# Performance work log

Hardware: AMD Instinct MI355X
Metric: run time of the kernel (lower is better)

## Reference

```python
import jax, jax.numpy as jnp
import numpy as np

N_NODES = 131072
N_EDGES = 2097152
N_GRAPHS = 2048
IN_CH, HID, OUT = 12, 64, 4


def gcn_conv(x, W, b, src, dst, n_nodes):
    """PyG GCNConv: out = D^{-1/2} (A + I) D^{-1/2} (x W) + b.
    Degree computed at target nodes including self loops (edge_weight=1)."""
    h = x @ W  # [N, F_out]
    # degree with self loops: in-degree + 1
    deg = jax.ops.segment_sum(jnp.ones((src.shape[0],), x.dtype), dst,
                              num_segments=n_nodes) + 1.0
    dinv = jax.lax.rsqrt(deg)  # [N]
    norm = dinv[src] * dinv[dst]  # [E]
    # scatter-add messages from src to dst
    agg = jax.ops.segment_sum(h[src] * norm[:, None], dst, num_segments=n_nodes)
    # self-loop contribution: norm_ii = dinv[i]^2
    agg = agg + h * (dinv * dinv)[:, None]
    return agg + b


def global_mean_pool(x, batch, n_graphs):
    sums = jax.ops.segment_sum(x, batch, num_segments=n_graphs)
    cnt = jax.ops.segment_sum(jnp.ones((x.shape[0],), x.dtype), batch,
                              num_segments=n_graphs)
    return sums / jnp.maximum(cnt, 1.0)[:, None]


def setup_inputs() -> dict:
    key = jax.random.key(0)
    ks = jax.random.split(key, 9)
    x = jax.random.normal(ks[0], (N_NODES, IN_CH), dtype=jnp.float32)
    edge_index = jax.random.randint(ks[1], (2, N_EDGES), 0, N_NODES, dtype=jnp.int64)
    batch = jnp.sort(jax.random.randint(ks[2], (N_NODES,), 0, N_GRAPHS, dtype=jnp.int64))
    def glorot(k, shape):
        lim = np.sqrt(6.0 / (shape[0] + shape[1]))
        return jax.random.uniform(k, shape, jnp.float32, -lim, lim)
    return {
        "x": x,
        "edge_index": edge_index,
        "batch": batch,
        "W1": glorot(ks[3], (IN_CH, HID)),
        "b1": jnp.zeros((HID,), jnp.float32),
        "W2": glorot(ks[4], (HID, HID)),
        "b2": jnp.zeros((HID,), jnp.float32),
        "Wfc": glorot(ks[5], (HID, OUT)),
        "bfc": jnp.zeros((OUT,), jnp.float32),
    }


def reference(x, edge_index, batch, W1, b1, W2, b2, Wfc, bfc):
    src, dst = edge_index[0], edge_index[1]
    h = jax.nn.relu(gcn_conv(x, W1, b1, src, dst, N_NODES))
    h = jax.nn.relu(gcn_conv(h, W2, b2, src, dst, N_NODES))
    g = global_mean_pool(h, batch, N_GRAPHS)  # [n_graphs, HID]
    return jax.nn.sigmoid(g @ Wfc + bfc)  # [n_graphs, OUT]
```

## Files before the change

### kernel.cpp

```cpp
#include <hip/hip_runtime.h>
#include <hip/hip_bf16.h>


#define N_NODES 131072
#define N_EDGES 2097152
#define N_GRAPHS 2048
#define IN_CH 12
#define HID 64
#define OUT_CH 4
#define NBUCK 512
#define CHUNK 8192
#define STRIDE 4608
#define CSR_STRIDE 5120
#define CAP 5120

typedef float f32x2 __attribute__((ext_vector_type(2)));

__global__ __launch_bounds__(1024, 4)
void bucket_kernel(const int* __restrict__ src, const int* __restrict__ dst,
                   int* __restrict__ bucket_count, int* __restrict__ staged) {
    __shared__ int hist[NBUCK];
    __shared__ int lscan[NBUCK];
    __shared__ int gbase[NBUCK];
    __shared__ int cursor[NBUCK];
    __shared__ int sorted[CHUNK];
    int tid = threadIdx.x;
    int base = blockIdx.x * CHUNK;
    if (tid < NBUCK) { hist[tid] = 0; cursor[tid] = 0; }
    __syncthreads();
    int d8[8], s8[8];
#pragma unroll
    for (int k = 0; k < 8; k++) {
        int i = base + k * 1024 + tid;
        d8[k] = dst[i];
        s8[k] = src[i];
        atomicAdd(&hist[d8[k] >> 8], 1);
    }
    __syncthreads();
    if (tid < NBUCK) lscan[tid] = hist[tid];
    __syncthreads();
    for (int off = 1; off < NBUCK; off <<= 1) {
        int u = (tid < NBUCK && tid >= off) ? lscan[tid - off] : 0;
        __syncthreads();
        if (tid < NBUCK) lscan[tid] += u;
        __syncthreads();
    }
    if (tid < NBUCK) gbase[tid] = atomicAdd(&bucket_count[tid], hist[tid]);
    __syncthreads();
#pragma unroll
    for (int k = 0; k < 8; k++) {
        int b = d8[k] >> 8;
        int start = lscan[b] - hist[b];
        int p = start + atomicAdd(&cursor[b], 1);
        sorted[p] = ((d8[k] & 255) << 17) | s8[k];
    }
    __syncthreads();
    int wid = tid >> 6, lane = tid & 63;
    int g16 = lane >> 4, k16 = lane & 15;
    for (int b0 = wid * 4; b0 < NBUCK; b0 += 64) {
        int b = b0 + g16;
        int cb = hist[b];
        int lbase = lscan[b] - cb;
        int gb = b * STRIDE + gbase[b];
        for (int k = k16; k < cb; k += 16) staged[gb + k] = sorted[lbase + k];
    }
}

__global__ void build_kernel(const int* __restrict__ bucket_count, const int* __restrict__ staged,
                             int2* __restrict__ rowbounds, float* __restrict__ dinv,
                             int* __restrict__ csr, const float* __restrict__ x,
                             uint4* __restrict__ xb) {
    __shared__ int sl[STRIDE];
    __shared__ int image[CAP];
    __shared__ int cnt[256];
    __shared__ int scn[256];
    __shared__ int loff[256];
    __shared__ int cursor[256];
    __shared__ int totalS;
    int b = blockIdx.x;
    int tid = threadIdx.x;
    int count = bucket_count[b];
    const int* st = staged + b * STRIDE;
    cnt[tid] = 0;
    cursor[tid] = 0;
    for (int i = tid; i < count; i += 256) sl[i] = st[i];
    __syncthreads();
    for (int i = tid; i < count; i += 256) atomicAdd(&cnt[(sl[i] >> 17) & 255], 1);
    __syncthreads();
    int deg = cnt[tid];
    int degp = (deg + 3) & ~3;
    scn[tid] = degp;
    __syncthreads();
    for (int off = 1; off < 256; off <<= 1) {
        int u = (tid >= off) ? scn[tid - off] : 0;
        __syncthreads();
        scn[tid] += u;
        __syncthreads();
    }
    int lo = scn[tid] - degp;
    loff[tid] = lo;
    int nbase = (b << 8) + tid;
    int gb = b * CSR_STRIDE;
    rowbounds[nbase] = make_int2(gb + lo, gb + lo + degp);
    float dv = rsqrtf((float)deg + 1.0f);
    dinv[nbase] = dv;
    if (tid == 255) totalS = lo + degp;
    {
        const float* xp = x + nbase * IN_CH;
        unsigned o0 = (unsigned)__builtin_amdgcn_cvt_pk_fp8_f32(dv * xp[0], dv * xp[1], 0, false);
        o0 = (unsigned)__builtin_amdgcn_cvt_pk_fp8_f32(dv * xp[2], dv * xp[3], (int)o0, true);
        unsigned o1 = (unsigned)__builtin_amdgcn_cvt_pk_fp8_f32(dv * xp[4], dv * xp[5], 0, false);
        o1 = (unsigned)__builtin_amdgcn_cvt_pk_fp8_f32(dv * xp[6], dv * xp[7], (int)o1, true);
        unsigned o2 = (unsigned)__builtin_amdgcn_cvt_pk_fp8_f32(dv * xp[8], dv * xp[9], 0, false);
        o2 = (unsigned)__builtin_amdgcn_cvt_pk_fp8_f32(dv * xp[10], dv * xp[11], (int)o2, true);
        xb[nbase] = make_uint4(o0, o1, o2, 0);
    }
    if (b == 0 && tid == 0)
        xb[N_NODES] = make_uint4(0, 0, 0, 0);
    __syncthreads();
    for (int i = tid; i < count; i += 256) {
        int rec = sl[i];
        int s = rec & 0x1FFFF;
        int dq = (rec >> 17) & 255;
        int p = loff[dq] + atomicAdd(&cursor[dq], 1);
        int val = s << 6;
        if (p < CAP) image[p] = val;
        else csr[gb + p] = val;
    }
    __syncthreads();
    int padval = N_NODES << 6;
    for (int p = loff[tid] + deg; p < loff[tid] + degp; p++) {
        if (p < CAP) image[p] = padval;
        else csr[gb + p] = padval;
    }
    __syncthreads();
    int lim = totalS < CAP ? totalS : CAP;
    int* dstp = csr + gb;
    for (int i = tid; i < lim; i += 256) dstp[i] = image[i];
}

__device__ __forceinline__ void accq2(f32x2* a, uint2 u) {
    a[0] += __builtin_amdgcn_cvt_pk_f32_fp8((int)u.x, false);
    a[1] += __builtin_amdgcn_cvt_pk_f32_fp8((int)u.x, true);
    a[2] += __builtin_amdgcn_cvt_pk_f32_fp8((int)u.y, false);
    a[3] += __builtin_amdgcn_cvt_pk_f32_fp8((int)u.y, true);
}

__global__ __launch_bounds__(256, 6)
void w1w2_kernel(const int2* __restrict__ rowbounds, const int* __restrict__ csr,
                 const float* __restrict__ dinv, const unsigned char* __restrict__ xb,
                 const float* __restrict__ W1, const float* __restrict__ b1,
                 const float* __restrict__ W2, unsigned int* __restrict__ hout) {
    __shared__ float sA[64 * 13];
    __shared__ float sh1t[HID * 65];
    int tid = threadIdx.x;
    int node0 = blockIdx.x * 64;
    {
        int nl = tid >> 2;
        int node = node0 + nl;
        int p = tid & 1, boff = 8 * p;
        int2 rb = rowbounds[node];
        float dn = dinv[node];
        uint2 su = {0, 0};
        if (!(tid & 2)) su = *(const uint2*)(xb + node * 16 + boff);
        int len = rb.y - rb.x;
        int hlen = (len >> 3) << 2;
        int beg = (tid & 2) ? rb.x + hlen : rb.x;
        int end = (tid & 2) ? rb.y : rb.x + hlen;
        f32x2 a0[4] = {{0, 0}, {0, 0}, {0, 0}, {0, 0}};
        f32x2 a1[4] = {{0, 0}, {0, 0}, {0, 0}, {0, 0}};
        int j = beg;
        for (; j + 8 <= end; j += 8) {
            int4 ea = *(const int4*)(csr + j);
            int4 eb = *(const int4*)(csr + j + 4);
            uint2 u0 = *(const uint2*)(xb + (ea.x >> 2) + boff);
            uint2 u1 = *(const uint2*)(xb + (ea.y >> 2) + boff);
            uint2 u2 = *(const uint2*)(xb + (ea.z >> 2) + boff);
            uint2 u3 = *(const uint2*)(xb + (ea.w >> 2) + boff);
            uint2 u4 = *(const uint2*)(xb + (eb.x >> 2) + boff);
            uint2 u5 = *(const uint2*)(xb + (eb.y >> 2) + boff);
            uint2 u6 = *(const uint2*)(xb + (eb.z >> 2) + boff);
            uint2 u7 = *(const uint2*)(xb + (eb.w >> 2) + boff);
            accq2(a0, u0); accq2(a1, u1); accq2(a0, u2); accq2(a1, u3);
            accq2(a0, u4); accq2(a1, u5); accq2(a0, u6); accq2(a1, u7);
        }
        if (j < end) {
            int4 ea = *(const int4*)(csr + j);
            uint2 u0 = *(const uint2*)(xb + (ea.x >> 2) + boff);
            uint2 u1 = *(const uint2*)(xb + (ea.y >> 2) + boff);
            uint2 u2 = *(const uint2*)(xb + (ea.z >> 2) + boff);
            uint2 u3 = *(const uint2*)(xb + (ea.w >> 2) + boff);
            accq2(a0, u0); accq2(a1, u1); accq2(a0, u2); accq2(a1, u3);
        }
        f32x2 s0 = a0[0] + a1[0];
        f32x2 s1 = a0[1] + a1[1];
        f32x2 s2 = a0[2] + a1[2];
        f32x2 s3 = a0[3] + a1[3];
        s0[0] += __shfl_xor(s0[0], 2); s0[1] += __shfl_xor(s0[1], 2);
        s1[0] += __shfl_xor(s1[0], 2); s1[1] += __shfl_xor(s1[1], 2);
        s2[0] += __shfl_xor(s2[0], 2); s2[1] += __shfl_xor(s2[1], 2);
        s3[0] += __shfl_xor(s3[0], 2); s3[1] += __shfl_xor(s3[1], 2);
        if (!(tid & 2)) {
            s0 += __builtin_amdgcn_cvt_pk_f32_fp8((int)su.x, false);
            s1 += __builtin_amdgcn_cvt_pk_f32_fp8((int)su.x, true);
            s2 += __builtin_amdgcn_cvt_pk_f32_fp8((int)su.y, false);
            s3 += __builtin_amdgcn_cvt_pk_f32_fp8((int)su.y, true);
            float* dp = &sA[nl * 13 + 8 * p];
            dp[0] = dn * s0[0]; dp[1] = dn * s0[1];
            dp[2] = dn * s1[0]; dp[3] = dn * s1[1];
            if (p == 0) {
                dp[4] = dn * s2[0]; dp[5] = dn * s2[1];
                dp[6] = dn * s3[0]; dp[7] = dn * s3[1];
            }
        }
    }
    __syncthreads();
    int w = tid >> 6, c = tid & 63;
    float bc = b1[c];
    float wk[IN_CH];
#pragma unroll
    for (int k = 0; k < IN_CH; k++) wk[k] = W1[k * HID + c];
#pragma unroll
    for (int it = 0; it < 4; it++) {
        int n0 = w * 16 + it * 4;
        float a0 = bc, a1 = bc, a2 = bc, a3 = bc;
#pragma unroll
        for (int k = 0; k < IN_CH; k++) {
            float wv = wk[k];
            a0 += sA[(n0 + 0) * 13 + k] * wv;
            a1 += sA[(n0 + 1) * 13 + k] * wv;
            a2 += sA[(n0 + 2) * 13 + k] * wv;
            a3 += sA[(n0 + 3) * 13 + k] * wv;
        }
        float4 o = make_float4(fmaxf(a0, 0.0f), fmaxf(a1, 0.0f),
                               fmaxf(a2, 0.0f), fmaxf(a3, 0.0f));
        *(float4*)&sh1t[c * 65 + n0] = o;
    }
    __syncthreads();
    int nq = tid >> 4, c4 = (tid & 15) * 4;
    float4 a0 = {0, 0, 0, 0}, a1 = {0, 0, 0, 0}, a2 = {0, 0, 0, 0}, a3 = {0, 0, 0, 0};
#pragma unroll 4
    for (int k = 0; k < HID; k++) {
        float4 wv = *(const float4*)&W2[k * HID + c4];
        float4 hv = *(const float4*)&sh1t[k * 65 + nq * 4];
        a0.x += hv.x * wv.x; a0.y += hv.x * wv.y; a0.z += hv.x * wv.z; a0.w += hv.x * wv.w;
        a1.x += hv.y * wv.x; a1.y += hv.y * wv.y; a1.z += hv.y * wv.z; a1.w += hv.y * wv.w;
        a2.x += hv.z * wv.x; a2.y += hv.z * wv.y; a2.z += hv.z * wv.z; a2.w += hv.z * wv.w;
        a3.x += hv.w * wv.x; a3.y += hv.w * wv.y; a3.z += hv.w * wv.z; a3.w += hv.w * wv.w;
    }
    int nb = node0 + nq * 4;
    float dv0 = dinv[nb + 0], dv1 = dinv[nb + 1], dv2 = dinv[nb + 2], dv3 = dinv[nb + 3];
    unsigned int p0 = (unsigned int)__builtin_amdgcn_cvt_pk_fp8_f32(dv0 * a0.x, dv0 * a0.y, 0, false);
    p0 = (unsigned int)__builtin_amdgcn_cvt_pk_fp8_f32(dv0 * a0.z, dv0 * a0.w, (int)p0, true);
    unsigned int p1 = (unsigned int)__builtin_amdgcn_cvt_pk_fp8_f32(dv1 * a1.x, dv1 * a1.y, 0, false);
    p1 = (unsigned int)__builtin_amdgcn_cvt_pk_fp8_f32(dv1 * a1.z, dv1 * a1.w, (int)p1, true);
    unsigned int p2 = (unsigned int)__builtin_amdgcn_cvt_pk_fp8_f32(dv2 * a2.x, dv2 * a2.y, 0, false);
    p2 = (unsigned int)__builtin_amdgcn_cvt_pk_fp8_f32(dv2 * a2.z, dv2 * a2.w, (int)p2, true);
    unsigned int p3 = (unsigned int)__builtin_amdgcn_cvt_pk_fp8_f32(dv3 * a3.x, dv3 * a3.y, 0, false);
    p3 = (unsigned int)__builtin_amdgcn_cvt_pk_fp8_f32(dv3 * a3.z, dv3 * a3.w, (int)p3, true);
    int cl = c4 >> 2;
    hout[(nb + 0) * 16 + cl] = p0;
    hout[(nb + 1) * 16 + cl] = p1;
    hout[(nb + 2) * 16 + cl] = p2;
    hout[(nb + 3) * 16 + cl] = p3;
    if (blockIdx.x == 0 && tid < 16)
        hout[(size_t)N_NODES * 16 + tid] = 0;
}

__device__ __forceinline__ void add_fp8q(f32x2* a, uint4 u) {
    a[0] += __builtin_amdgcn_cvt_pk_f32_fp8((int)u.x, false);
    a[1] += __builtin_amdgcn_cvt_pk_f32_fp8((int)u.x, true);
    a[2] += __builtin_amdgcn_cvt_pk_f32_fp8((int)u.y, false);
    a[3] += __builtin_amdgcn_cvt_pk_f32_fp8((int)u.y, true);
    a[4] += __builtin_amdgcn_cvt_pk_f32_fp8((int)u.z, false);
    a[5] += __builtin_amdgcn_cvt_pk_f32_fp8((int)u.z, true);
    a[6] += __builtin_amdgcn_cvt_pk_f32_fp8((int)u.w, false);
    a[7] += __builtin_amdgcn_cvt_pk_f32_fp8((int)u.w, true);
}

__device__ __forceinline__ void agg_body16(int beg, int end, const int* __restrict__ csr,
                                           const unsigned char* __restrict__ h,
                                           int qoff, float* r) {
    f32x2 a0[8] = {{0, 0}, {0, 0}, {0, 0}, {0, 0}, {0, 0}, {0, 0}, {0, 0}, {0, 0}};
    f32x2 a1[8] = {{0, 0}, {0, 0}, {0, 0}, {0, 0}, {0, 0}, {0, 0}, {0, 0}, {0, 0}};
    int j = beg;
    for (; j + 8 <= end; j += 8) {
        int4 ea = *(const int4*)(csr + j);
        int4 eb = *(const int4*)(csr + j + 4);
        uint4 u0 = *(const uint4*)(h + ea.x + qoff);
        uint4 u1 = *(const uint4*)(h + ea.y + qoff);
        uint4 u2 = *(const uint4*)(h + ea.z + qoff);
        uint4 u3 = *(const uint4*)(h + ea.w + qoff);
        uint4 u4 = *(const uint4*)(h + eb.x + qoff);
        uint4 u5 = *(const uint4*)(h + eb.y + qoff);
        uint4 u6 = *(const uint4*)(h + eb.z + qoff);
        uint4 u7 = *(const uint4*)(h + eb.w + qoff);
        add_fp8q(a0, u0); add_fp8q(a1, u1); add_fp8q(a0, u2); add_fp8q(a1, u3);
        add_fp8q(a0, u4); add_fp8q(a1, u5); add_fp8q(a0, u6); add_fp8q(a1, u7);
    }
    if (j < end) {
        int4 ea = *(const int4*)(csr + j);
        uint4 u0 = *(const uint4*)(h + ea.x + qoff);
        uint4 u1 = *(const uint4*)(h + ea.y + qoff);
        uint4 u2 = *(const uint4*)(h + ea.z + qoff);
        uint4 u3 = *(const uint4*)(h + ea.w + qoff);
        add_fp8q(a0, u0); add_fp8q(a1, u1); add_fp8q(a0, u2); add_fp8q(a1, u3);
    }
#pragma unroll
    for (int k = 0; k < 8; k++) {
        f32x2 s = a0[k] + a1[k];
        r[2 * k] = s[0];
        r[2 * k + 1] = s[1];
    }
}

__global__ void agg_pool_kernel(const int2* __restrict__ rowbounds, const int* __restrict__ csr,
                                const float* __restrict__ dinv,
                                const unsigned char* __restrict__ h,
                                const float* __restrict__ b, const int* __restrict__ batch,
                                float* __restrict__ pool, float* __restrict__ gcnt) {
    __shared__ float red[64][HID + 4];
    __shared__ int gids[64];
    int tid = threadIdx.x;
    int w = tid >> 6, lane = tid & 63, sub = lane >> 2, q = lane & 3;
    int qoff = 16 * q;
    int node = (blockIdx.x * 4 + w) * 16 + sub;
    int2 rb = rowbounds[node];
    float dn = dinv[node];
    uint4 su = *(const uint4*)(h + node * HID + qoff);
    int gid = batch[node];
    float r[16];
    agg_body16(rb.x, rb.y, csr, h, qoff, r);
    f32x2 s[8];
    s[0] = __builtin_amdgcn_cvt_pk_f32_fp8((int)su.x, false);
    s[1] = __builtin_amdgcn_cvt_pk_f32_fp8((int)su.x, true);
    s[2] = __builtin_amdgcn_cvt_pk_f32_fp8((int)su.y, false);
    s[3] = __builtin_amdgcn_cvt_pk_f32_fp8((int)su.y, true);
    s[4] = __builtin_amdgcn_cvt_pk_f32_fp8((int)su.z, false);
    s[5] = __builtin_amdgcn_cvt_pk_f32_fp8((int)su.z, true);
    s[6] = __builtin_amdgcn_cvt_pk_f32_fp8((int)su.w, false);
    s[7] = __builtin_amdgcn_cvt_pk_f32_fp8((int)su.w, true);
    int nl = w * 16 + sub;
    float* rp = &red[nl][qoff];
#pragma unroll
    for (int k = 0; k < 4; k++) {
        float4 bv = *(const float4*)&b[qoff + 4 * k];
        rp[4 * k + 0] = fmaxf(dn * (r[4 * k + 0] + s[2 * k][0]) + bv.x, 0.0f);
        rp[4 * k + 1] = fmaxf(dn * (r[4 * k + 1] + s[2 * k][1]) + bv.y, 0.0f);
        rp[4 * k + 2] = fmaxf(dn * (r[4 * k + 2] + s[2 * k + 1][0]) + bv.z, 0.0f);
        rp[4 * k + 3] = fmaxf(dn * (r[4 * k + 3] + s[2 * k + 1][1]) + bv.w, 0.0f);
    }
    if (q == 0) gids[nl] = gid;
    __syncthreads();
    if (tid < 64) {
        int c = tid;
        float acc = 0.0f;
        int cur = gids[0], cnt = 0;
        for (int n = 0; n < 64; n++) {
            int g = gids[n];
            if (g != cur) {
                atomicAdd(&pool[cur * HID + c], acc);
                if (c == 0) atomicAdd(&gcnt[cur], (float)cnt);
                acc = 0.0f; cnt = 0; cur = g;
            }
            acc += red[n][c];
            cnt++;
        }
        atomicAdd(&pool[cur * HID + c], acc);
        if (c == 0) atomicAdd(&gcnt[cur], (float)cnt);
    }
}

__global__ void final_kernel(const float* __restrict__ pool, const float* __restrict__ gcnt,
                             const float* __restrict__ Wfc, const float* __restrict__ bfc,
                             float* __restrict__ out) {
    int idx = blockIdx.x * 256 + threadIdx.x;
    if (idx >= N_GRAPHS * OUT_CH) return;
    int g = idx >> 2, o = idx & 3;
    float inv = 1.0f / fmaxf(gcnt[g], 1.0f);
    float acc = bfc[o];
#pragma unroll
    for (int k = 0; k < HID; k++) acc += pool[g * HID + k] * inv * Wfc[k * OUT_CH + o];
    out[idx] = 1.0f / (1.0f + expf(-acc));
}

extern "C" void kernel_launch(void* const* d_in, const int* in_sizes, int n_in,
                              void* d_out, int out_size, void* d_ws, size_t ws_size,
                              hipStream_t stream) {
    const float* x   = (const float*)d_in[0];
    const int* eidx  = (const int*)d_in[1];
    const int* batch = (const int*)d_in[2];
    const float* W1  = (const float*)d_in[3];
    const float* b1  = (const float*)d_in[4];
    const float* W2  = (const float*)d_in[5];
    const float* b2  = (const float*)d_in[6];
    const float* Wfc = (const float*)d_in[7];
    const float* bfc = (const float*)d_in[8];
    float* out = (float*)d_out;

    const int* src = eidx;
    const int* dst = eidx + N_EDGES;

    unsigned char* hB = (unsigned char*)d_ws;
    int*   csr    = (int*)(hB + (size_t)(N_NODES + 1) * HID);
    int*   staged = csr + (size_t)NBUCK * CSR_STRIDE;
    float* dinv   = (float*)(staged + (size_t)NBUCK * STRIDE);
    int2*  rowbounds = (int2*)(dinv + N_NODES);
    int*   bucket_count = (int*)(rowbounds + N_NODES);
    float* pool   = (float*)(bucket_count + NBUCK);
    float* gcnt   = pool + N_GRAPHS * HID;
    uint4* xb     = (uint4*)(gcnt + N_GRAPHS);

    hipMemsetAsync(bucket_count, 0,
                   (size_t)(NBUCK + N_GRAPHS * HID + N_GRAPHS) * 4, stream);

    bucket_kernel<<<N_EDGES / CHUNK, 1024, 0, stream>>>(src, dst, bucket_count, staged);
    build_kernel<<<NBUCK, 256, 0, stream>>>(bucket_count, staged, rowbounds, dinv, csr, x, xb);

    w1w2_kernel<<<N_NODES / 64, 256, 0, stream>>>(rowbounds, csr, dinv,
                                                  (const unsigned char*)xb, W1, b1, W2,
                                                  (unsigned int*)hB);

    agg_pool_kernel<<<N_NODES / 64, 256, 0, stream>>>(rowbounds, csr, dinv, hB, b2, batch,
                                                      pool, gcnt);

    final_kernel<<<(N_GRAPHS * OUT_CH + 255) / 256, 256, 0, stream>>>(pool, gcnt, Wfc, bfc, out);
}
```

Measured before the change: 178.2 us.

## Split CSR rows by source half and switch layer-1 gather to full 12-byte rows

The CSR build now splits each destination row into two sub-segments by one bit of the source index, each padded to 4, and records the split point in a new rowmid array. The aggregation kernel walks the two segments in turn, which probably groups gathers into nearby source regions for better cache locality. The layer-1 gather now lets each of four lanes load a whole 16-byte fp8 row per edge, striding over edge groups, instead of splitting features across lanes. The costs are extra padding, a larger CSR stride, one extra metadata load per node, and more shuffles in the reduction.

```diff
diff --git a/kernel.cpp b/kernel.cpp
--- a/kernel.cpp
+++ b/kernel.cpp
@@ -11,8 +11,8 @@
 #define NBUCK 512
 #define CHUNK 8192
 #define STRIDE 4608
-#define CSR_STRIDE 5120
-#define CAP 5120
+#define CSR_STRIDE 5632
+#define CAP 5632
 
 typedef float f32x2 __attribute__((ext_vector_type(2)));
 
@@ -67,28 +67,37 @@
 }
 
 __global__ void build_kernel(const int* __restrict__ bucket_count, const int* __restrict__ staged,
-                             int2* __restrict__ rowbounds, float* __restrict__ dinv,
+                             int2* __restrict__ rowbounds, int* __restrict__ rowmid,
+                             float* __restrict__ dinv,
                              int* __restrict__ csr, const float* __restrict__ x,
                              uint4* __restrict__ xb) {
     __shared__ int sl[STRIDE];
     __shared__ int image[CAP];
-    __shared__ int cnt[256];
+    __shared__ int cnt[512];
+    __shared__ int cursor[512];
     __shared__ int scn[256];
-    __shared__ int loff[256];
-    __shared__ int cursor[256];
+    __shared__ int loffA[256];
+    __shared__ int loffB[256];
     __shared__ int totalS;
     int b = blockIdx.x;
     int tid = threadIdx.x;
     int count = bucket_count[b];
     const int* st = staged + b * STRIDE;
-    cnt[tid] = 0;
-    cursor[tid] = 0;
+    cnt[tid] = 0; cnt[tid + 256] = 0;
+    cursor[tid] = 0; cursor[tid + 256] = 0;
     for (int i = tid; i < count; i += 256) sl[i] = st[i];
     __syncthreads();
-    for (int i = tid; i < count; i += 256) atomicAdd(&cnt[(sl[i] >> 17) & 255], 1);
-    __syncthreads();
-    int deg = cnt[tid];
-    int degp = (deg + 3) & ~3;
+    for (int i = tid; i < count; i += 256) {
+        int rec = sl[i];
+        int dq = (rec >> 17) & 255;
+        int half = (rec >> 16) & 1;
+        atomicAdd(&cnt[(dq << 1) | half], 1);
+    }
+    __syncthreads();
+    int degA = cnt[tid << 1], degB = cnt[(tid << 1) | 1];
+    int degpA = (degA + 3) & ~3, degpB = (degB + 3) & ~3;
+    int degp = degpA + degpB;
+    int deg = degA + degB;
     scn[tid] = degp;
     __syncthreads();
     for (int off = 1; off < 256; off <<= 1) {
@@ -98,10 +107,12 @@
         __syncthreads();
     }
     int lo = scn[tid] - degp;
-    loff[tid] = lo;
+    loffA[tid] = lo;
+    loffB[tid] = lo + degpA;
     int nbase = (b << 8) + tid;
     int gb = b * CSR_STRIDE;
     rowbounds[nbase] = make_int2(gb + lo, gb + lo + degp);
+    rowmid[nbase] = gb + lo + degpA;
     float dv = rsqrtf((float)deg + 1.0f);
     dinv[nbase] = dv;
     if (tid == 255) totalS = lo + degp;
@@ -122,14 +133,20 @@
         int rec = sl[i];
         int s = rec & 0x1FFFF;
         int dq = (rec >> 17) & 255;
-        int p = loff[dq] + atomicAdd(&cursor[dq], 1);
+        int half = (rec >> 16) & 1;
+        int base0 = half ? loffB[dq] : loffA[dq];
+        int p = base0 + atomicAdd(&cursor[(dq << 1) | half], 1);
         int val = s << 6;
         if (p < CAP) image[p] = val;
         else csr[gb + p] = val;
     }
     __syncthreads();
     int padval = N_NODES << 6;
-    for (int p = loff[tid] + deg; p < loff[tid] + degp; p++) {
+    for (int p = loffA[tid] + degA; p < loffA[tid] + degpA; p++) {
+        if (p < CAP) image[p] = padval;
+        else csr[gb + p] = padval;
+    }
+    for (int p = loffB[tid] + degB; p < loffB[tid] + degpB; p++) {
         if (p < CAP) image[p] = padval;
         else csr[gb + p] = padval;
     }
@@ -139,11 +156,13 @@
     for (int i = tid; i < lim; i += 256) dstp[i] = image[i];
 }
 
-__device__ __forceinline__ void accq2(f32x2* a, uint2 u) {
+__device__ __forceinline__ void acc12(f32x2* a, uint4 u) {
     a[0] += __builtin_amdgcn_cvt_pk_f32_fp8((int)u.x, false);
     a[1] += __builtin_amdgcn_cvt_pk_f32_fp8((int)u.x, true);
     a[2] += __builtin_amdgcn_cvt_pk_f32_fp8((int)u.y, false);
     a[3] += __builtin_amdgcn_cvt_pk_f32_fp8((int)u.y, true);
+    a[4] += __builtin_amdgcn_cvt_pk_f32_fp8((int)u.z, false);
+    a[5] += __builtin_amdgcn_cvt_pk_f32_fp8((int)u.z, true);
 }
 
 __global__ __launch_bounds__(256, 6)
@@ -158,60 +177,45 @@
     {
         int nl = tid >> 2;
         int node = node0 + nl;
-        int p = tid & 1, boff = 8 * p;
+        int t = tid & 3;
         int2 rb = rowbounds[node];
         float dn = dinv[node];
-        uint2 su = {0, 0};
-        if (!(tid & 2)) su = *(const uint2*)(xb + node * 16 + boff);
-        int len = rb.y - rb.x;
-        int hlen = (len >> 3) << 2;
-        int beg = (tid & 2) ? rb.x + hlen : rb.x;
-        int end = (tid & 2) ? rb.y : rb.x + hlen;
-        f32x2 a0[4] = {{0, 0}, {0, 0}, {0, 0}, {0, 0}};
-        f32x2 a1[4] = {{0, 0}, {0, 0}, {0, 0}, {0, 0}};
-        int j = beg;
-        for (; j + 8 <= end; j += 8) {
-            int4 ea = *(const int4*)(csr + j);
-            int4 eb = *(const int4*)(csr + j + 4);
-            uint2 u0 = *(const uint2*)(xb + (ea.x >> 2) + boff);
-            uint2 u1 = *(const uint2*)(xb + (ea.y >> 2) + boff);
-            uint2 u2 = *(const uint2*)(xb + (ea.z >> 2) + boff);
-            uint2 u3 = *(const uint2*)(xb + (ea.w >> 2) + boff);
-            uint2 u4 = *(const uint2*)(xb + (eb.x >> 2) + boff);
-            uint2 u5 = *(const uint2*)(xb + (eb.y >> 2) + boff);
-            uint2 u6 = *(const uint2*)(xb + (eb.z >> 2) + boff);
-            uint2 u7 = *(const uint2*)(xb + (eb.w >> 2) + boff);
-            accq2(a0, u0); accq2(a1, u1); accq2(a0, u2); accq2(a1, u3);
-            accq2(a0, u4); accq2(a1, u5); accq2(a0, u6); accq2(a1, u7);
+        uint4 su = make_uint4(0, 0, 0, 0);
+        if (t == 0) su = *(const uint4*)(xb + node * 16);
+        int m = (rb.y - rb.x) >> 2;
+        f32x2 a0[6] = {{0,0},{0,0},{0,0},{0,0},{0,0},{0,0}};
+        f32x2 a1[6] = {{0,0},{0,0},{0,0},{0,0},{0,0},{0,0}};
+#pragma unroll 2
+        for (int g = t; g < m; g += 4) {
+            int4 e = *(const int4*)(csr + rb.x + 4 * g);
+            uint4 r0 = *(const uint4*)(xb + (e.x >> 2));
+            uint4 r1 = *(const uint4*)(xb + (e.y >> 2));
+            uint4 r2 = *(const uint4*)(xb + (e.z >> 2));
+            uint4 r3 = *(const uint4*)(xb + (e.w >> 2));
+            acc12(a0, r0); acc12(a1, r1); acc12(a0, r2); acc12(a1, r3);
         }
-        if (j < end) {
-            int4 ea = *(const int4*)(csr + j);
-            uint2 u0 = *(const uint2*)(xb + (ea.x >> 2) + boff);
-            uint2 u1 = *(const uint2*)(xb + (ea.y >> 2) + boff);
-            uint2 u2 = *(const uint2*)(xb + (ea.z >> 2) + boff);
-            uint2 u3 = *(const uint2*)(xb + (ea.w >> 2) + boff);
-            accq2(a0, u0); accq2(a1, u1); accq2(a0, u2); accq2(a1, u3);
+        float sv[12];
+#pragma unroll
+        for (int k = 0; k < 6; k++) {
+            f32x2 v = a0[k] + a1[k];
+            v[0] += __shfl_xor(v[0], 1); v[1] += __shfl_xor(v[1], 1);
+            v[0] += __shfl_xor(v[0], 2); v[1] += __shfl_xor(v[1], 2);
+            sv[2 * k] = v[0]; sv[2 * k + 1] = v[1];
         }
-        f32x2 s0 = a0[0] + a1[0];
-        f32x2 s1 = a0[1] + a1[1];
-        f32x2 s2 = a0[2] + a1[2];
-        f32x2 s3 = a0[3] + a1[3];
-        s0[0] += __shfl_xor(s0[0], 2); s0[1] += __shfl_xor(s0[1], 2);
-        s1[0] += __shfl_xor(s1[0], 2); s1[1] += __shfl_xor(s1[1], 2);
-        s2[0] += __shfl_xor(s2[0], 2); s2[1] += __shfl_xor(s2[1], 2);
-        s3[0] += __shfl_xor(s3[0], 2); s3[1] += __shfl_xor(s3[1], 2);
-        if (!(tid & 2)) {
-            s0 += __builtin_amdgcn_cvt_pk_f32_fp8((int)su.x, false);
-            s1 += __builtin_amdgcn_cvt_pk_f32_fp8((int)su.x, true);
-            s2 += __builtin_amdgcn_cvt_pk_f32_fp8((int)su.y, false);
-            s3 += __builtin_amdgcn_cvt_pk_f32_fp8((int)su.y, true);
-            float* dp = &sA[nl * 13 + 8 * p];
-            dp[0] = dn * s0[0]; dp[1] = dn * s0[1];
-            dp[2] = dn * s1[0]; dp[3] = dn * s1[1];
-            if (p == 0) {
-                dp[4] = dn * s2[0]; dp[5] = dn * s2[1];
-                dp[6] = dn * s3[0]; dp[7] = dn * s3[1];
-            }
+        if (t == 0) {
+            f32x2 q0 = __builtin_amdgcn_cvt_pk_f32_fp8((int)su.x, false);
+            f32x2 q1 = __builtin_amdgcn_cvt_pk_f32_fp8((int)su.x, true);
+            f32x2 q2 = __builtin_amdgcn_cvt_pk_f32_fp8((int)su.y, false);
+            f32x2 q3 = __builtin_amdgcn_cvt_pk_f32_fp8((int)su.y, true);
+            f32x2 q4 = __builtin_amdgcn_cvt_pk_f32_fp8((int)su.z, false);
+            f32x2 q5 = __builtin_amdgcn_cvt_pk_f32_fp8((int)su.z, true);
+            float* dp = &sA[nl * 13];
+            dp[0]  = dn * (sv[0]  + q0[0]); dp[1]  = dn * (sv[1]  + q0[1]);
+            dp[2]  = dn * (sv[2]  + q1[0]); dp[3]  = dn * (sv[3]  + q1[1]);
+            dp[4]  = dn * (sv[4]  + q2[0]); dp[5]  = dn * (sv[5]  + q2[1]);
+            dp[6]  = dn * (sv[6]  + q3[0]); dp[7]  = dn * (sv[7]  + q3[1]);
+            dp[8]  = dn * (sv[8]  + q4[0]); dp[9]  = dn * (sv[9]  + q4[1]);
+            dp[10] = dn * (sv[10] + q5[0]); dp[11] = dn * (sv[11] + q5[1]);
         }
     }
     __syncthreads();
@@ -278,11 +282,9 @@
     a[7] += __builtin_amdgcn_cvt_pk_f32_fp8((int)u.w, true);
 }
 
-__device__ __forceinline__ void agg_body16(int beg, int end, const int* __restrict__ csr,
-                                           const unsigned char* __restrict__ h,
-                                           int qoff, float* r) {
-    f32x2 a0[8] = {{0, 0}, {0, 0}, {0, 0}, {0, 0}, {0, 0}, {0, 0}, {0, 0}, {0, 0}};
-    f32x2 a1[8] = {{0, 0}, {0, 0}, {0, 0}, {0, 0}, {0, 0}, {0, 0}, {0, 0}, {0, 0}};
+__device__ __forceinline__ void agg_seg(int beg, int end, const int* __restrict__ csr,
+                                        const unsigned char* __restrict__ h,
+                                        int qoff, f32x2* a0, f32x2* a1) {
     int j = beg;
     for (; j + 8 <= end; j += 8) {
         int4 ea = *(const int4*)(csr + j);
@@ -306,15 +308,10 @@
         uint4 u3 = *(const uint4*)(h + ea.w + qoff);
         add_fp8q(a0, u0); add_fp8q(a1, u1); add_fp8q(a0, u2); add_fp8q(a1, u3);
     }
-#pragma unroll
-    for (int k = 0; k < 8; k++) {
-        f32x2 s = a0[k] + a1[k];
-        r[2 * k] = s[0];
-        r[2 * k + 1] = s[1];
-    }
-}
-
-__global__ void agg_pool_kernel(const int2* __restrict__ rowbounds, const int* __restrict__ csr,
+}
+
+__global__ void agg_pool_kernel(const int2* __restrict__ rowbounds, const int* __restrict__ rowmid,
+                                const int* __restrict__ csr,
                                 const float* __restrict__ dinv,
                                 const unsigned char* __restrict__ h,
                                 const float* __restrict__ b, const int* __restrict__ batch,
@@ -326,11 +323,21 @@
     int qoff = 16 * q;
     int node = (blockIdx.x * 4 + w) * 16 + sub;
     int2 rb = rowbounds[node];
+    int mid = rowmid[node];
     float dn = dinv[node];
     uint4 su = *(const uint4*)(h + node * HID + qoff);
     int gid = batch[node];
+    f32x2 a0[8] = {{0,0},{0,0},{0,0},{0,0},{0,0},{0,0},{0,0},{0,0}};
+    f32x2 a1[8] = {{0,0},{0,0},{0,0},{0,0},{0,0},{0,0},{0,0},{0,0}};
+    agg_seg(rb.x, mid, csr, h, qoff, a0, a1);
+    agg_seg(mid, rb.y, csr, h, qoff, a0, a1);
     float r[16];
-    agg_body16(rb.x, rb.y, csr, h, qoff, r);
+#pragma unroll
+    for (int k = 0; k < 8; k++) {
+        f32x2 s2 = a0[k] + a1[k];
+        r[2 * k] = s2[0];
+        r[2 * k + 1] = s2[1];
+    }
     f32x2 s[8];
     s[0] = __builtin_amdgcn_cvt_pk_f32_fp8((int)su.x, false);
     s[1] = __builtin_amdgcn_cvt_pk_f32_fp8((int)su.x, true);
@@ -406,7 +413,8 @@
     int*   staged = csr + (size_t)NBUCK * CSR_STRIDE;
     float* dinv   = (float*)(staged + (size_t)NBUCK * STRIDE);
     int2*  rowbounds = (int2*)(dinv + N_NODES);
-    int*   bucket_count = (int*)(rowbounds + N_NODES);
+    int*   rowmid = (int*)(rowbounds + N_NODES);
+    int*   bucket_count = (int*)(rowmid + N_NODES);
     float* pool   = (float*)(bucket_count + NBUCK);
     float* gcnt   = pool + N_GRAPHS * HID;
     uint4* xb     = (uint4*)(gcnt + N_GRAPHS);
@@ -415,14 +423,15 @@
                    (size_t)(NBUCK + N_GRAPHS * HID + N_GRAPHS) * 4, stream);
 
     bucket_kernel<<<N_EDGES / CHUNK, 1024, 0, stream>>>(src, dst, bucket_count, staged);
-    build_kernel<<<NBUCK, 256, 0, stream>>>(bucket_count, staged, rowbounds, dinv, csr, x, xb);
+    build_kernel<<<NBUCK, 256, 0, stream>>>(bucket_count, staged, rowbounds, rowmid,
+                                            dinv, csr, x, xb);
 
     w1w2_kernel<<<N_NODES / 64, 256, 0, stream>>>(rowbounds, csr, dinv,
                                                   (const unsigned char*)xb, W1, b1, W2,
                                                   (unsigned int*)hB);
 
-    agg_pool_kernel<<<N_NODES / 64, 256, 0, stream>>>(rowbounds, csr, dinv, hB, b2, batch,
-                                                      pool, gcnt);
+    agg_pool_kernel<<<N_NODES / 64, 256, 0, stream>>>(rowbounds, rowmid, csr, dinv, hB, b2,
+                                                      batch, pool, gcnt);
 
     final_kernel<<<(N_GRAPHS * OUT_CH + 255) / 256, 256, 0, stream>>>(pool, gcnt, Wfc, bfc, out);
 }
```

After: 187.5 us. +5.2%, slower.

## Split fp8 hidden table into two 32-channel halves for cache-local gather

Applied to the files above, without the earlier changes.

The layer-2 fp8 feature table is split into two separate 32-byte-per-node tables, one per half of the channels. The aggregation kernel now processes one half per block, with 2 threads per node, and interleaves block indices so both halves of neighbouring node ranges run close together. The goal is to halve the working set each gather touches so it fits better in L2/MALL. The cost is that the CSR and row bounds are read twice and there are twice as many pooling atomics.

```diff
diff --git a/kernel.cpp b/kernel.cpp
--- a/kernel.cpp
+++ b/kernel.cpp
@@ -13,6 +13,7 @@
 #define STRIDE 4608
 #define CSR_STRIDE 5120
 #define CAP 5120
+#define TBLW ((N_NODES + 1) * 8)
 
 typedef float f32x2 __attribute__((ext_vector_type(2)));
 
@@ -259,12 +260,14 @@
     unsigned int p3 = (unsigned int)__builtin_amdgcn_cvt_pk_fp8_f32(dv3 * a3.x, dv3 * a3.y, 0, false);
     p3 = (unsigned int)__builtin_amdgcn_cvt_pk_fp8_f32(dv3 * a3.z, dv3 * a3.w, (int)p3, true);
     int cl = c4 >> 2;
-    hout[(nb + 0) * 16 + cl] = p0;
-    hout[(nb + 1) * 16 + cl] = p1;
-    hout[(nb + 2) * 16 + cl] = p2;
-    hout[(nb + 3) * 16 + cl] = p3;
+    int t = cl >> 3;
+    unsigned int* hw = hout + (size_t)t * TBLW + (cl & 7);
+    hw[(nb + 0) * 8] = p0;
+    hw[(nb + 1) * 8] = p1;
+    hw[(nb + 2) * 8] = p2;
+    hw[(nb + 3) * 8] = p3;
     if (blockIdx.x == 0 && tid < 16)
-        hout[(size_t)N_NODES * 16 + tid] = 0;
+        hout[(size_t)(tid >> 3) * TBLW + (size_t)N_NODES * 8 + (tid & 7)] = 0;
 }
 
 __device__ __forceinline__ void add_fp8q(f32x2* a, uint4 u) {
@@ -278,59 +281,63 @@
     a[7] += __builtin_amdgcn_cvt_pk_f32_fp8((int)u.w, true);
 }
 
-__device__ __forceinline__ void agg_body16(int beg, int end, const int* __restrict__ csr,
-                                           const unsigned char* __restrict__ h,
-                                           int qoff, float* r) {
-    f32x2 a0[8] = {{0, 0}, {0, 0}, {0, 0}, {0, 0}, {0, 0}, {0, 0}, {0, 0}, {0, 0}};
-    f32x2 a1[8] = {{0, 0}, {0, 0}, {0, 0}, {0, 0}, {0, 0}, {0, 0}, {0, 0}, {0, 0}};
+__device__ __forceinline__ void agg_seg2(int beg, int end, const int* __restrict__ csr,
+                                         const unsigned char* __restrict__ h,
+                                         int qoff, f32x2* a0, f32x2* a1) {
     int j = beg;
     for (; j + 8 <= end; j += 8) {
         int4 ea = *(const int4*)(csr + j);
         int4 eb = *(const int4*)(csr + j + 4);
-        uint4 u0 = *(const uint4*)(h + ea.x + qoff);
-        uint4 u1 = *(const uint4*)(h + ea.y + qoff);
-        uint4 u2 = *(const uint4*)(h + ea.z + qoff);
-        uint4 u3 = *(const uint4*)(h + ea.w + qoff);
-        uint4 u4 = *(const uint4*)(h + eb.x + qoff);
-        uint4 u5 = *(const uint4*)(h + eb.y + qoff);
-        uint4 u6 = *(const uint4*)(h + eb.z + qoff);
-        uint4 u7 = *(const uint4*)(h + eb.w + qoff);
+        uint4 u0 = *(const uint4*)(h + (ea.x >> 1) + qoff);
+        uint4 u1 = *(const uint4*)(h + (ea.y >> 1) + qoff);
+        uint4 u2 = *(const uint4*)(h + (ea.z >> 1) + qoff);
+        uint4 u3 = *(const uint4*)(h + (ea.w >> 1) + qoff);
+        uint4 u4 = *(const uint4*)(h + (eb.x >> 1) + qoff);
+        uint4 u5 = *(const uint4*)(h + (eb.y >> 1) + qoff);
+        uint4 u6 = *(const uint4*)(h + (eb.z >> 1) + qoff);
+        uint4 u7 = *(const uint4*)(h + (eb.w >> 1) + qoff);
         add_fp8q(a0, u0); add_fp8q(a1, u1); add_fp8q(a0, u2); add_fp8q(a1, u3);
         add_fp8q(a0, u4); add_fp8q(a1, u5); add_fp8q(a0, u6); add_fp8q(a1, u7);
     }
     if (j < end) {
         int4 ea = *(const int4*)(csr + j);
-        uint4 u0 = *(const uint4*)(h + ea.x + qoff);
-        uint4 u1 = *(const uint4*)(h + ea.y + qoff);
-        uint4 u2 = *(const uint4*)(h + ea.z + qoff);
-        uint4 u3 = *(const uint4*)(h + ea.w + qoff);
+        uint4 u0 = *(const uint4*)(h + (ea.x >> 1) + qoff);
+        uint4 u1 = *(const uint4*)(h + (ea.y >> 1) + qoff);
+        uint4 u2 = *(const uint4*)(h + (ea.z >> 1) + qoff);
+        uint4 u3 = *(const uint4*)(h + (ea.w >> 1) + qoff);
         add_fp8q(a0, u0); add_fp8q(a1, u1); add_fp8q(a0, u2); add_fp8q(a1, u3);
-    }
-#pragma unroll
-    for (int k = 0; k < 8; k++) {
-        f32x2 s = a0[k] + a1[k];
-        r[2 * k] = s[0];
-        r[2 * k + 1] = s[1];
     }
 }
 
 __global__ void agg_pool_kernel(const int2* __restrict__ rowbounds, const int* __restrict__ csr,
                                 const float* __restrict__ dinv,
-                                const unsigned char* __restrict__ h,
+                                const unsigned int* __restrict__ hbase,
                                 const float* __restrict__ b, const int* __restrict__ batch,
                                 float* __restrict__ pool, float* __restrict__ gcnt) {
-    __shared__ float red[64][HID + 4];
-    __shared__ int gids[64];
+    __shared__ float red[128][36];
+    __shared__ int gids[128];
     int tid = threadIdx.x;
-    int w = tid >> 6, lane = tid & 63, sub = lane >> 2, q = lane & 3;
+    int xq = blockIdx.x & 7;
+    int half = xq >> 2;
+    int nbb = ((blockIdx.x >> 3) << 2) | (xq & 3);
+    int nl = tid >> 1, q = tid & 1;
+    int node = nbb * 128 + nl;
+    const unsigned char* h = (const unsigned char*)(hbase + (size_t)half * TBLW);
     int qoff = 16 * q;
-    int node = (blockIdx.x * 4 + w) * 16 + sub;
     int2 rb = rowbounds[node];
     float dn = dinv[node];
-    uint4 su = *(const uint4*)(h + node * HID + qoff);
+    uint4 su = *(const uint4*)(h + node * 32 + qoff);
     int gid = batch[node];
+    f32x2 a0[8] = {{0,0},{0,0},{0,0},{0,0},{0,0},{0,0},{0,0},{0,0}};
+    f32x2 a1[8] = {{0,0},{0,0},{0,0},{0,0},{0,0},{0,0},{0,0},{0,0}};
+    agg_seg2(rb.x, rb.y, csr, h, qoff, a0, a1);
     float r[16];
-    agg_body16(rb.x, rb.y, csr, h, qoff, r);
+#pragma unroll
+    for (int k = 0; k < 8; k++) {
+        f32x2 s2 = a0[k] + a1[k];
+        r[2 * k] = s2[0];
+        r[2 * k + 1] = s2[1];
+    }
     f32x2 s[8];
     s[0] = __builtin_amdgcn_cvt_pk_f32_fp8((int)su.x, false);
     s[1] = __builtin_amdgcn_cvt_pk_f32_fp8((int)su.x, true);
@@ -340,11 +347,11 @@
     s[5] = __builtin_amdgcn_cvt_pk_f32_fp8((int)su.z, true);
     s[6] = __builtin_amdgcn_cvt_pk_f32_fp8((int)su.w, false);
     s[7] = __builtin_amdgcn_cvt_pk_f32_fp8((int)su.w, true);
-    int nl = w * 16 + sub;
-    float* rp = &red[nl][qoff];
+    int cbase = half * 32 + q * 16;
+    float* rp = &red[nl][q * 16];
 #pragma unroll
     for (int k = 0; k < 4; k++) {
-        float4 bv = *(const float4*)&b[qoff + 4 * k];
+        float4 bv = *(const float4*)&b[cbase + 4 * k];
         rp[4 * k + 0] = fmaxf(dn * (r[4 * k + 0] + s[2 * k][0]) + bv.x, 0.0f);
         rp[4 * k + 1] = fmaxf(dn * (r[4 * k + 1] + s[2 * k][1]) + bv.y, 0.0f);
         rp[4 * k + 2] = fmaxf(dn * (r[4 * k + 2] + s[2 * k + 1][0]) + bv.z, 0.0f);
@@ -353,21 +360,22 @@
     if (q == 0) gids[nl] = gid;
     __syncthreads();
     if (tid < 64) {
-        int c = tid;
+        int c = tid & 31;
+        int n0 = (tid >> 5) * 64;
         float acc = 0.0f;
-        int cur = gids[0], cnt = 0;
-        for (int n = 0; n < 64; n++) {
+        int cur = gids[n0], cnt = 0;
+        for (int n = n0; n < n0 + 64; n++) {
             int g = gids[n];
             if (g != cur) {
-                atomicAdd(&pool[cur * HID + c], acc);
-                if (c == 0) atomicAdd(&gcnt[cur], (float)cnt);
+                atomicAdd(&pool[cur * HID + half * 32 + c], acc);
+                if (c == 0 && half == 0) atomicAdd(&gcnt[cur], (float)cnt);
                 acc = 0.0f; cnt = 0; cur = g;
             }
             acc += red[n][c];
             cnt++;
         }
-        atomicAdd(&pool[cur * HID + c], acc);
-        if (c == 0) atomicAdd(&gcnt[cur], (float)cnt);
+        atomicAdd(&pool[cur * HID + half * 32 + c], acc);
+        if (c == 0 && half == 0) atomicAdd(&gcnt[cur], (float)cnt);
     }
 }
 
@@ -401,8 +409,8 @@
     const int* src = eidx;
     const int* dst = eidx + N_EDGES;
 
-    unsigned char* hB = (unsigned char*)d_ws;
-    int*   csr    = (int*)(hB + (size_t)(N_NODES + 1) * HID);
+    unsigned int* hB = (unsigned int*)d_ws;
+    int*   csr    = (int*)(hB + 2 * (size_t)TBLW);
     int*   staged = csr + (size_t)NBUCK * CSR_STRIDE;
     float* dinv   = (float*)(staged + (size_t)NBUCK * STRIDE);
     int2*  rowbounds = (int2*)(dinv + N_NODES);
@@ -418,11 +426,10 @@
     build_kernel<<<NBUCK, 256, 0, stream>>>(bucket_count, staged, rowbounds, dinv, csr, x, xb);
 
     w1w2_kernel<<<N_NODES / 64, 256, 0, stream>>>(rowbounds, csr, dinv,
-                                                  (const unsigned char*)xb, W1, b1, W2,
-                                                  (unsigned int*)hB);
-
-    agg_pool_kernel<<<N_NODES / 64, 256, 0, stream>>>(rowbounds, csr, dinv, hB, b2, batch,
-                                                      pool, gcnt);
+                                                  (const unsigned char*)xb, W1, b1, W2, hB);
+
+    agg_pool_kernel<<<(N_NODES / 128) * 2, 256, 0, stream>>>(rowbounds, csr, dinv, hB, b2,
+                                                             batch, pool, gcnt);
 
     final_kernel<<<(N_GRAPHS * OUT_CH + 255) / 256, 256, 0, stream>>>(pool, gcnt, Wfc, bfc, out);
 }
```

New measurement: 184.0 us. 3.3% more time.
